# Optimization experiments

Measured on AMD Instinct MI355X. Metric: run time of the kernel, lower is better.

Reference implementation:

```python
import jax, jax.numpy as jnp
import numpy as np

N = 50000
E = 600000
IN_CH = 128
HID = 64


def setup_inputs() -> dict:
    key = jax.random.key(0)
    ks = jax.random.split(key, 8)
    x = jax.random.normal(ks[0], (N, IN_CH), dtype=jnp.float32)
    edge_index = jax.random.randint(ks[1], (2, E), 0, N, dtype=jnp.int64)
    s = 1.0 / np.sqrt(IN_CH)
    W_rel = jax.random.uniform(ks[2], (IN_CH, HID), jnp.float32, -s, s)
    b_rel = jax.random.uniform(ks[3], (HID,), jnp.float32, -s, s)
    W_root = jax.random.uniform(ks[4], (IN_CH, HID), jnp.float32, -s, s)
    sh = 1.0 / np.sqrt(HID)
    W_dec = jax.random.uniform(ks[5], (HID, IN_CH), jnp.float32, -sh, sh)
    b_dec = jax.random.uniform(ks[6], (IN_CH,), jnp.float32, -sh, sh)
    return {"x": x, "edge_index": edge_index, "W_rel": W_rel, "b_rel": b_rel,
            "W_root": W_root, "W_dec": W_dec, "b_dec": b_dec}


def reference(x, edge_index, W_rel, b_rel, W_root, W_dec, b_dec):
    src, dst = edge_index[0], edge_index[1]
    # gather source node features, sum-aggregate at destination nodes  [N, IN_CH]
    agg = jax.ops.segment_sum(x[src], dst, num_segments=N)
    # GraphConv: lin_rel(agg) + lin_root(x)  (lin_rel carries the bias)
    h = agg @ W_rel + b_rel + x @ W_root
    h = jax.nn.relu(h)
    # linear decoder back to input feature space
    return h @ W_dec + b_dec
```

## Files before the change

### kernel.cpp

```cpp
#include <hip/hip_runtime.h>

#define IN_CH 128
#define HID 64
#define ELLW 32
#define SPILLCAP 4096
#define NSCAT 256
#define BCAP 3584

typedef short v8s __attribute__((ext_vector_type(8)));
typedef float v4f __attribute__((ext_vector_type(4)));

__device__ __forceinline__ unsigned int bf16pair(float a, float b) {
    unsigned int ua = __float_as_uint(a);
    unsigned int ub = __float_as_uint(b);
    ua = (ua + 0x7fffu + ((ua >> 16) & 1u)) >> 16;
    ub = (ub + 0x7fffu + ((ub >> 16) & 1u)) & 0xffff0000u;
    return ua | ub;
}
__device__ __forceinline__ unsigned short bf16of(float a) {
    unsigned int ua = __float_as_uint(a);
    return (unsigned short)((ua + 0x7fffu + ((ua >> 16) & 1u)) >> 16);
}

__global__ __launch_bounds__(256) void graphmae_prep(
    const float* __restrict__ W_rel, const float* __restrict__ W_root,
    unsigned short* __restrict__ Bt, int* __restrict__ bucketcur, int NZ)
{
    const int idx = blockIdx.x * 256 + threadIdx.x;
    if (idx < NZ) bucketcur[idx] = 0;
    const int k = idx >> 7;
    const int c = idx & 127;
    const float v = (c < HID) ? W_rel[(size_t)k * HID + c]
                              : W_root[(size_t)k * HID + (c - HID)];
    Bt[(size_t)c * 128 + k] = bf16of(v);
}

__global__ __launch_bounds__(512) void graphmae_encode_scatter(
    const float* __restrict__ x, const unsigned short* __restrict__ Bt,
    const float* __restrict__ b_rel, const int* __restrict__ ei,
    unsigned short* __restrict__ y16, float* __restrict__ agg,
    int* __restrict__ bucketcur, unsigned int* __restrict__ sorted,
    int* __restrict__ spillcnt, int2* __restrict__ spill,
    int N, int E, int NBUK, int CE)
{
    __shared__ int lh[256];
    __shared__ int lcur[256];

    const int t  = threadIdx.x;
    const int n0 = blockIdx.x * 64;
    const bool sduty = (blockIdx.x < NSCAT);
    const int e0 = blockIdx.x * CE;
    const int e1 = sduty ? min(E, e0 + CE) : 0;

    if (t >= 256) { lh[t - 256] = 0; lcur[t - 256] = 0; }
    __syncthreads();

    if (t < 256) {
        const int w    = t >> 6;
        const int lane = t & 63;
        const int mr   = lane & 15;
        const int kg   = lane >> 4;
        const int nrow = n0 + w * 16 + mr;

        v8s afrag[4];
        #pragma unroll
        for (int ks = 0; ks < 4; ++ks) {
            uint4 pk = make_uint4(0u, 0u, 0u, 0u);
            if (nrow < N) {
                const float* xp = x + (size_t)nrow * IN_CH + ks * 32 + kg * 8;
                const float4 u0 = *(const float4*)(xp);
                const float4 u1 = *(const float4*)(xp + 4);
                pk = make_uint4(bf16pair(u0.x, u0.y), bf16pair(u0.z, u0.w),
                                bf16pair(u1.x, u1.y), bf16pair(u1.z, u1.w));
            }
            afrag[ks] = *(v8s*)&pk;
        }

        const int rbase = n0 + w * 16 + kg * 4;
        #pragma unroll
        for (int ct = 0; ct < 8; ++ct) {
            v4f acc = {0.f, 0.f, 0.f, 0.f};
            const unsigned short* bp = Bt + (size_t)(ct * 16 + mr) * 128 + kg * 8;
            #pragma unroll
            for (int ks = 0; ks < 4; ++ks) {
                const v8s b = *(const v8s*)(bp + ks * 32);
                acc = __builtin_amdgcn_mfma_f32_16x16x32_bf16(afrag[ks], b, acc, 0, 0, 0);
            }
            const int c = ct * 16 + mr;
            if (ct < 4) {
                #pragma unroll
                for (int r = 0; r < 4; ++r) {
                    const int n = rbase + r;
                    if (n < N) y16[(size_t)n * HID + c] = bf16of(acc[r]);
                }
            } else {
                const float br = b_rel[c - HID];
                #pragma unroll
                for (int r = 0; r < 4; ++r) {
                    const int n = rbase + r;
                    if (n < N) agg[(size_t)n * HID + (c - HID)] = acc[r] + br;
                }
            }
        }
    } else if (sduty) {
        for (int e = e0 + (t - 256); e < e1; e += 256)
            atomicAdd(&lh[ei[E + e] >> 8], 1);
    }
    __syncthreads();

    if (t >= 256 && sduty) {
        const int b = t - 256;
        if (b < NBUK) {
            const int cnt = lh[b];
            if (cnt > 0) lcur[b] = atomicAdd(&bucketcur[b], cnt);
        }
    }
    __syncthreads();

    if (t >= 256 && sduty) {
        for (int e = e0 + (t - 256); e < e1; e += 256) {
            const int d = ei[E + e];
            const int s = ei[e];
            const int b = d >> 8;
            const int pos = atomicAdd(&lcur[b], 1);
            if (pos < BCAP) {
                sorted[(size_t)b * BCAP + pos] =
                    ((unsigned)(d & 255) << 16) | (unsigned)s;
            } else {
                const int p = atomicAdd(spillcnt, 1);
                if (p < SPILLCAP) spill[p] = make_int2(d, s);
            }
        }
    }
}

__global__ __launch_bounds__(256) void bucket_fill(
    const unsigned int* __restrict__ sorted, const int* __restrict__ bucketcur,
    int* __restrict__ deg, unsigned short* __restrict__ slots16,
    int* __restrict__ spillcnt, int2* __restrict__ spill)
{
    __shared__ int cnt[256];
    __shared__ unsigned short sl[256 * ELLW];
    const int t = threadIdx.x, b = blockIdx.x;
    cnt[t] = 0;
    __syncthreads();

    const int m = min(bucketcur[b], BCAP);
    const unsigned int* src = sorted + (size_t)b * BCAP;
    for (int i = t; i < m; i += 256) {
        const unsigned int v = src[i];
        const int dl = v >> 16;
        const int r = atomicAdd(&cnt[dl], 1);
        if (r < ELLW) sl[dl * ELLW + r] = (unsigned short)(v & 0xffffu);
        else {
            const int p = atomicAdd(spillcnt, 1);
            if (p < SPILLCAP) spill[p] = make_int2((b << 8) + dl, (int)(v & 0xffffu));
        }
    }
    __syncthreads();

    deg[(b << 8) + t] = cnt[t];
    unsigned int* g = (unsigned int*)slots16 + (size_t)b * 4096;
    const unsigned int* l = (const unsigned int*)sl;
    for (int i = t; i < 4096; i += 256) g[i] = l[i];
}

__global__ __launch_bounds__(256) void graphmae_gather(
    const int* __restrict__ deg, const unsigned short* __restrict__ slots16,
    const unsigned short* __restrict__ y16, const float* __restrict__ agg,
    const int* __restrict__ spillcnt, const int2* __restrict__ spill,
    unsigned short* __restrict__ h16, int N)
{
    const int n = blockIdx.x * 4 + (threadIdx.x >> 6);
    if (n >= N) return;
    const int lane = threadIdx.x & 63;
    const int es   = lane >> 3;
    const int cl   = lane & 7;

    const int cnt = min(deg[n], ELLW);
    const unsigned short* sp = slots16 + (size_t)n * ELLW;

    float4 a0 = make_float4(0.f, 0.f, 0.f, 0.f);
    float4 a1 = make_float4(0.f, 0.f, 0.f, 0.f);
    if (es == 0) {
        a0 = *(const float4*)(agg + (size_t)n * HID + cl * 8);
        a1 = *(const float4*)(agg + (size_t)n * HID + cl * 8 + 4);
    }

    float acc[8];
    #pragma unroll
    for (int j = 0; j < 8; ++j) acc[j] = 0.f;

    for (int e = es; e < cnt; e += 8) {
        const int s = sp[e];
        const uint4 v = *(const uint4*)(y16 + (size_t)s * HID + cl * 8);
        acc[0] += __uint_as_float(v.x << 16);
        acc[1] += __uint_as_float(v.x & 0xffff0000u);
        acc[2] += __uint_as_float(v.y << 16);
        acc[3] += __uint_as_float(v.y & 0xffff0000u);
        acc[4] += __uint_as_float(v.z << 16);
        acc[5] += __uint_as_float(v.z & 0xffff0000u);
        acc[6] += __uint_as_float(v.w << 16);
        acc[7] += __uint_as_float(v.w & 0xffff0000u);
    }

    const int spN = min(*spillcnt, SPILLCAP);
    for (int i = es; i < spN; i += 8) {
        const int2 e2 = spill[i];
        if (e2.x == n) {
            const uint4 v = *(const uint4*)(y16 + (size_t)e2.y * HID + cl * 8);
            acc[0] += __uint_as_float(v.x << 16);
            acc[1] += __uint_as_float(v.x & 0xffff0000u);
            acc[2] += __uint_as_float(v.y << 16);
            acc[3] += __uint_as_float(v.y & 0xffff0000u);
            acc[4] += __uint_as_float(v.z << 16);
            acc[5] += __uint_as_float(v.z & 0xffff0000u);
            acc[6] += __uint_as_float(v.w << 16);
            acc[7] += __uint_as_float(v.w & 0xffff0000u);
        }
    }

    #pragma unroll
    for (int m = 8; m <= 32; m <<= 1) {
        #pragma unroll
        for (int j = 0; j < 8; ++j) acc[j] += __shfl_xor(acc[j], m);
    }

    if (es == 0) {
        const float h0 = fmaxf(a0.x + acc[0], 0.f);
        const float h1 = fmaxf(a0.y + acc[1], 0.f);
        const float h2 = fmaxf(a0.z + acc[2], 0.f);
        const float h3 = fmaxf(a0.w + acc[3], 0.f);
        const float h4 = fmaxf(a1.x + acc[4], 0.f);
        const float h5 = fmaxf(a1.y + acc[5], 0.f);
        const float h6 = fmaxf(a1.z + acc[6], 0.f);
        const float h7 = fmaxf(a1.w + acc[7], 0.f);
        uint4 o;
        o.x = bf16pair(h0, h1);
        o.y = bf16pair(h2, h3);
        o.z = bf16pair(h4, h5);
        o.w = bf16pair(h6, h7);
        *(uint4*)(h16 + (size_t)n * HID + cl * 8) = o;
    }
}

__global__ __launch_bounds__(256) void graphmae_decode(
    const unsigned short* __restrict__ h16, const float* __restrict__ W_dec,
    const float* __restrict__ b_dec, float* __restrict__ out, int N)
{
    __shared__ unsigned short As[64][72];
    __shared__ unsigned short Bs[128][72];

    const int t  = threadIdx.x;
    const int n0 = blockIdx.x * 64;

    {
        const int r = t >> 2, q = t & 3;
        const int n = n0 + r;
        unsigned short* ap = &As[r][q * 16];
        if (n < N) {
            const unsigned short* hp = h16 + (size_t)n * HID + q * 16;
            #pragma unroll
            for (int j = 0; j < 4; ++j)
                *(uint2*)(ap + j * 4) = *(const uint2*)(hp + j * 4);
        } else {
            #pragma unroll
            for (int j = 0; j < 4; ++j) *(uint2*)(ap + j * 4) = make_uint2(0u, 0u);
        }
    }
    #pragma unroll
    for (int p = 0; p < 8; ++p) {
        const int idx = t + p * 256;
        const int k   = idx >> 5;
        const int c4  = (idx & 31) * 4;
        const float4 v = *(const float4*)(W_dec + (size_t)k * IN_CH + c4);
        Bs[c4 + 0][k] = bf16of(v.x);
        Bs[c4 + 1][k] = bf16of(v.y);
        Bs[c4 + 2][k] = bf16of(v.z);
        Bs[c4 + 3][k] = bf16of(v.w);
    }
    __syncthreads();

    const int w    = t >> 6;
    const int lane = t & 63;
    const int mr   = lane & 15;
    const int kg   = lane >> 4;

    v8s afrag[2];
    #pragma unroll
    for (int ks = 0; ks < 2; ++ks)
        afrag[ks] = *(const v8s*)(&As[w * 16 + mr][ks * 32 + kg * 8]);

    const int rbase = n0 + w * 16 + kg * 4;
    #pragma unroll
    for (int ct = 0; ct < 8; ++ct) {
        v4f acc = {0.f, 0.f, 0.f, 0.f};
        #pragma unroll
        for (int ks = 0; ks < 2; ++ks) {
            const v8s b = *(const v8s*)(&Bs[ct * 16 + mr][ks * 32 + kg * 8]);
            acc = __builtin_amdgcn_mfma_f32_16x16x32_bf16(afrag[ks], b, acc, 0, 0, 0);
        }
        const int c  = ct * 16 + mr;
        const float bd = b_dec[c];
        #pragma unroll
        for (int r = 0; r < 4; ++r) {
            const int n = rbase + r;
            if (n < N) out[(size_t)n * IN_CH + c] = acc[r] + bd;
        }
    }
}

extern "C" void kernel_launch(void* const* d_in, const int* in_sizes, int n_in,
                              void* d_out, int out_size, void* d_ws, size_t ws_size,
                              hipStream_t stream)
{
    const float* x      = (const float*)d_in[0];
    const int*   ei     = (const int*)  d_in[1];
    const float* W_rel  = (const float*)d_in[2];
    const float* b_rel  = (const float*)d_in[3];
    const float* W_root = (const float*)d_in[4];
    const float* W_dec  = (const float*)d_in[5];
    const float* b_dec  = (const float*)d_in[6];
    float* out = (float*)d_out;

    const int N = in_sizes[0] / IN_CH;
    const int E = in_sizes[1] / 2;

    const int NBUK = (N + 255) / 256;
    const int NPAD = NBUK * 256;
    const int CE   = (E + NSCAT - 1) / NSCAT;

    unsigned short* y16 = (unsigned short*)d_ws;
    float* agg          = (float*)(y16 + (size_t)N * HID);
    unsigned short* h16 = (unsigned short*)(agg + (size_t)N * HID);
    int* deg            = (int*)(h16 + (size_t)N * HID);
    unsigned short* slots16 = (unsigned short*)(deg + NPAD);
    unsigned int* sorted = (unsigned int*)(slots16 + (size_t)NPAD * ELLW);
    int* bucketcur = (int*)(sorted + (size_t)NBUK * BCAP);
    int* spillcnt  = bucketcur + NBUK;
    int2* spill    = (int2*)(spillcnt + 3);
    unsigned short* Bt = (unsigned short*)(spill + SPILLCAP);

    const int nblk64 = (N + 63) / 64;

    graphmae_prep<<<64, 256, 0, stream>>>(W_rel, W_root, Bt, bucketcur, NBUK + 1);

    graphmae_encode_scatter<<<nblk64, 512, 0, stream>>>(
        x, Bt, b_rel, ei, y16, agg,
        bucketcur, sorted, spillcnt, spill, N, E, NBUK, CE);

    bucket_fill<<<NBUK, 256, 0, stream>>>(sorted, bucketcur, deg, slots16,
                                          spillcnt, spill);

    const int gblk = (N + 3) / 4;
    graphmae_gather<<<gblk, 256, 0, stream>>>(deg, slots16, y16, agg,
                                              spillcnt, spill, h16, N);
    graphmae_decode<<<nblk64, 256, 0, stream>>>(h16, W_dec, b_dec, out, N);
}
```

Baseline: 83.38 us.

## Swap MFMA operands for vectorized row stores and pretranspose decoder weights once

The MFMA operand order in both encode and decode is swapped, so each lane holds four consecutive output columns of a single row. That lets results be written as vector stores (uint2/float4) instead of scattered scalar stores with a per-row stride. The decoder weight transpose and bf16 conversion move into the prep kernel and run once rather than in every decode block. This removes the decode kernel's shared memory and barrier, and decode now reads the weights directly from global memory.

Result: no change. 81.87 us (-1.8%).

```diff
diff --git a/kernel.cpp b/kernel.cpp
--- a/kernel.cpp
+++ b/kernel.cpp
@@ -24,15 +24,24 @@
 
 __global__ __launch_bounds__(256) void graphmae_prep(
     const float* __restrict__ W_rel, const float* __restrict__ W_root,
-    unsigned short* __restrict__ Bt, int* __restrict__ bucketcur, int NZ)
+    const float* __restrict__ W_dec,
+    unsigned short* __restrict__ Bt, unsigned short* __restrict__ Wdt,
+    int* __restrict__ bucketcur, int NZ)
 {
     const int idx = blockIdx.x * 256 + threadIdx.x;
     if (idx < NZ) bucketcur[idx] = 0;
-    const int k = idx >> 7;
-    const int c = idx & 127;
-    const float v = (c < HID) ? W_rel[(size_t)k * HID + c]
-                              : W_root[(size_t)k * HID + (c - HID)];
-    Bt[(size_t)c * 128 + k] = bf16of(v);
+    if (idx < 16384) {
+        const int k = idx >> 7;
+        const int c = idx & 127;
+        const float v = (c < HID) ? W_rel[(size_t)k * HID + c]
+                                  : W_root[(size_t)k * HID + (c - HID)];
+        Bt[(size_t)c * 128 + k] = bf16of(v);
+    } else if (idx < 24576) {
+        const int j = idx - 16384;
+        const int k = j >> 7;
+        const int c = j & 127;
+        Wdt[(size_t)c * 64 + k] = bf16of(W_dec[(size_t)k * IN_CH + c]);
+    }
 }
 
 __global__ __launch_bounds__(512) void graphmae_encode_scatter(
@@ -62,7 +71,7 @@
         const int kg   = lane >> 4;
         const int nrow = n0 + w * 16 + mr;
 
-        v8s afrag[4];
+        v8s xfrag[4];
         #pragma unroll
         for (int ks = 0; ks < 4; ++ks) {
             uint4 pk = make_uint4(0u, 0u, 0u, 0u);
@@ -73,10 +82,9 @@
                 pk = make_uint4(bf16pair(u0.x, u0.y), bf16pair(u0.z, u0.w),
                                 bf16pair(u1.x, u1.y), bf16pair(u1.z, u1.w));
             }
-            afrag[ks] = *(v8s*)&pk;
-        }
-
-        const int rbase = n0 + w * 16 + kg * 4;
+            xfrag[ks] = *(v8s*)&pk;
+        }
+
         #pragma unroll
         for (int ct = 0; ct < 8; ++ct) {
             v4f acc = {0.f, 0.f, 0.f, 0.f};
@@ -84,21 +92,19 @@
             #pragma unroll
             for (int ks = 0; ks < 4; ++ks) {
                 const v8s b = *(const v8s*)(bp + ks * 32);
-                acc = __builtin_amdgcn_mfma_f32_16x16x32_bf16(afrag[ks], b, acc, 0, 0, 0);
+                acc = __builtin_amdgcn_mfma_f32_16x16x32_bf16(b, xfrag[ks], acc, 0, 0, 0);
             }
-            const int c = ct * 16 + mr;
-            if (ct < 4) {
-                #pragma unroll
-                for (int r = 0; r < 4; ++r) {
-                    const int n = rbase + r;
-                    if (n < N) y16[(size_t)n * HID + c] = bf16of(acc[r]);
-                }
-            } else {
-                const float br = b_rel[c - HID];
-                #pragma unroll
-                for (int r = 0; r < 4; ++r) {
-                    const int n = rbase + r;
-                    if (n < N) agg[(size_t)n * HID + (c - HID)] = acc[r] + br;
+            if (nrow < N) {
+                if (ct < 4) {
+                    const int c = ct * 16 + kg * 4;
+                    *(uint2*)(y16 + (size_t)nrow * HID + c) =
+                        make_uint2(bf16pair(acc[0], acc[1]), bf16pair(acc[2], acc[3]));
+                } else {
+                    const int c = (ct - 4) * 16 + kg * 4;
+                    const float4 br = *(const float4*)(b_rel + c);
+                    *(float4*)(agg + (size_t)nrow * HID + c) =
+                        make_float4(acc[0] + br.x, acc[1] + br.y,
+                                    acc[2] + br.z, acc[3] + br.w);
                 }
             }
         }
@@ -245,67 +251,41 @@
 }
 
 __global__ __launch_bounds__(256) void graphmae_decode(
-    const unsigned short* __restrict__ h16, const float* __restrict__ W_dec,
+    const unsigned short* __restrict__ h16, const unsigned short* __restrict__ Wdt,
     const float* __restrict__ b_dec, float* __restrict__ out, int N)
 {
-    __shared__ unsigned short As[64][72];
-    __shared__ unsigned short Bs[128][72];
-
     const int t  = threadIdx.x;
     const int n0 = blockIdx.x * 64;
-
-    {
-        const int r = t >> 2, q = t & 3;
-        const int n = n0 + r;
-        unsigned short* ap = &As[r][q * 16];
-        if (n < N) {
-            const unsigned short* hp = h16 + (size_t)n * HID + q * 16;
-            #pragma unroll
-            for (int j = 0; j < 4; ++j)
-                *(uint2*)(ap + j * 4) = *(const uint2*)(hp + j * 4);
-        } else {
-            #pragma unroll
-            for (int j = 0; j < 4; ++j) *(uint2*)(ap + j * 4) = make_uint2(0u, 0u);
-        }
-    }
-    #pragma unroll
-    for (int p = 0; p < 8; ++p) {
-        const int idx = t + p * 256;
-        const int k   = idx >> 5;
-        const int c4  = (idx & 31) * 4;
-        const float4 v = *(const float4*)(W_dec + (size_t)k * IN_CH + c4);
-        Bs[c4 + 0][k] = bf16of(v.x);
-        Bs[c4 + 1][k] = bf16of(v.y);
-        Bs[c4 + 2][k] = bf16of(v.z);
-        Bs[c4 + 3][k] = bf16of(v.w);
-    }
-    __syncthreads();
-
     const int w    = t >> 6;
     const int lane = t & 63;
     const int mr   = lane & 15;
     const int kg   = lane >> 4;
-
-    v8s afrag[2];
+    const int nrow = n0 + w * 16 + mr;
+
+    v8s hfrag[2];
     #pragma unroll
-    for (int ks = 0; ks < 2; ++ks)
-        afrag[ks] = *(const v8s*)(&As[w * 16 + mr][ks * 32 + kg * 8]);
-
-    const int rbase = n0 + w * 16 + kg * 4;
+    for (int ks = 0; ks < 2; ++ks) {
+        uint4 pk = make_uint4(0u, 0u, 0u, 0u);
+        if (nrow < N)
+            pk = *(const uint4*)(h16 + (size_t)nrow * HID + ks * 32 + kg * 8);
+        hfrag[ks] = *(v8s*)&pk;
+    }
+
     #pragma unroll
     for (int ct = 0; ct < 8; ++ct) {
         v4f acc = {0.f, 0.f, 0.f, 0.f};
+        const unsigned short* wp = Wdt + (size_t)(ct * 16 + mr) * 64 + kg * 8;
         #pragma unroll
         for (int ks = 0; ks < 2; ++ks) {
-            const v8s b = *(const v8s*)(&Bs[ct * 16 + mr][ks * 32 + kg * 8]);
-            acc = __builtin_amdgcn_mfma_f32_16x16x32_bf16(afrag[ks], b, acc, 0, 0, 0);
-        }
-        const int c  = ct * 16 + mr;
-        const float bd = b_dec[c];
-        #pragma unroll
-        for (int r = 0; r < 4; ++r) {
-            const int n = rbase + r;
-            if (n < N) out[(size_t)n * IN_CH + c] = acc[r] + bd;
+            const v8s b = *(const v8s*)(wp + ks * 32);
+            acc = __builtin_amdgcn_mfma_f32_16x16x32_bf16(b, hfrag[ks], acc, 0, 0, 0);
+        }
+        if (nrow < N) {
+            const int c = ct * 16 + kg * 4;
+            const float4 bd = *(const float4*)(b_dec + c);
+            *(float4*)(out + (size_t)nrow * IN_CH + c) =
+                make_float4(acc[0] + bd.x, acc[1] + bd.y,
+                            acc[2] + bd.z, acc[3] + bd.w);
         }
     }
 }
@@ -339,11 +319,13 @@
     int* bucketcur = (int*)(sorted + (size_t)NBUK * BCAP);
     int* spillcnt  = bucketcur + NBUK;
     int2* spill    = (int2*)(spillcnt + 3);
-    unsigned short* Bt = (unsigned short*)(spill + SPILLCAP);
+    unsigned short* Bt  = (unsigned short*)(spill + SPILLCAP);
+    unsigned short* Wdt = Bt + 128 * 128;
 
     const int nblk64 = (N + 63) / 64;
 
-    graphmae_prep<<<64, 256, 0, stream>>>(W_rel, W_root, Bt, bucketcur, NBUK + 1);
+    graphmae_prep<<<96, 256, 0, stream>>>(W_rel, W_root, W_dec, Bt, Wdt,
+                                          bucketcur, NBUK + 1);
 
     graphmae_encode_scatter<<<nblk64, 512, 0, stream>>>(
         x, Bt, b_rel, ei, y16, agg,
@@ -355,5 +337,5 @@
     const int gblk = (N + 3) / 4;
     graphmae_gather<<<gblk, 256, 0, stream>>>(deg, slots16, y16, agg,
                                               spillcnt, spill, h16, N);
-    graphmae_decode<<<nblk64, 256, 0, stream>>>(h16, W_dec, b_dec, out, N);
-}
+    graphmae_decode<<<nblk64, 256, 0, stream>>>(h16, Wdt, b_dec, out, N);
+}
```
